# Performance work log

Hardware: AMD Instinct MI355X
Metric: run time of the kernel (lower is better)

The kernel has to match this reference:

```python
import jax, jax.numpy as jnp
import numpy as np

DEMBED = 512
DMODEL = 512
HEAD = 8
B, L = 4, 2048


def setup_inputs() -> dict:
    key = jax.random.key(0)
    ks = jax.random.split(key, 12)
    s_in = 1.0 / np.sqrt(DEMBED)
    s_out = 1.0 / np.sqrt(DMODEL)
    return {
        "x_q": jax.random.normal(ks[0], (B, L, DEMBED), jnp.float32),
        "x_k": jax.random.normal(ks[1], (B, L, DEMBED), jnp.float32),
        "x_v": jax.random.normal(ks[2], (B, L, DEMBED), jnp.float32),
        "mask": jax.random.randint(ks[3], (B, L, L), 0, 2, jnp.int32),
        "Wq": jax.random.uniform(ks[4], (DMODEL, DEMBED), jnp.float32, -s_in, s_in),
        "bq": jnp.zeros((DMODEL,), jnp.float32),
        "Wk": jax.random.uniform(ks[5], (DMODEL, DEMBED), jnp.float32, -s_in, s_in),
        "bk": jnp.zeros((DMODEL,), jnp.float32),
        "Wv": jax.random.uniform(ks[6], (DMODEL, DEMBED), jnp.float32, -s_in, s_in),
        "bv": jnp.zeros((DMODEL,), jnp.float32),
        "Wo": jax.random.uniform(ks[7], (DEMBED, DMODEL), jnp.float32, -s_out, s_out),
        "bo": jnp.zeros((DEMBED,), jnp.float32),
    }


def _split_heads(x):
    # [B, L, D] -> [B, head, L, h_dv]; head h gets contiguous channels h*h_dv:(h+1)*h_dv,
    # matching torch's transpose(1,2).reshape(B,head,h_dv,L).transpose(2,3)
    b, l, d = x.shape
    return x.reshape(b, l, HEAD, d // HEAD).transpose(0, 2, 1, 3)


def reference(x_q, x_k, x_v, mask, Wq, bq, Wk, bk, Wv, bv, Wo, bo):
    q = _split_heads(x_q @ Wq.T + bq)  # [B, H, L, hd]
    k = _split_heads(x_k @ Wk.T + bk)
    v = _split_heads(x_v @ Wv.T + bv)
    h_dv = q.shape[-1]
    scores = jnp.einsum("bhqd,bhkd->bhqk", q, k) / np.sqrt(h_dv)
    scores = scores + mask[:, None, :, :].astype(scores.dtype) * (-1e30)
    attn = jax.nn.softmax(scores, axis=-1)
    out = jnp.einsum("bhqk,bhkd->bhqd", attn, v)  # [B, H, L, hd]
    out = out.transpose(0, 2, 1, 3).reshape(x_q.shape[0], x_q.shape[1], DMODEL)
    final = out @ Wo.T + bo
    return final, attn
```

## Files before the change

kernel.cpp:

```cpp
#include <hip/hip_runtime.h>

typedef unsigned short u16;
typedef __attribute__((ext_vector_type(8))) short short8;
typedef __attribute__((ext_vector_type(4))) float f32x4;

#define DE 512
#define SL 2048
#define NB 4
#define NH 8
#define HD 64

__device__ __forceinline__ float bf2f(u16 h) {
    union { unsigned u; float f; } v; v.u = ((unsigned)h) << 16; return v.f;
}
__device__ __forceinline__ u16 f2bf(float f) {
    union { float f; unsigned u; } v; v.f = f;
    unsigned u = v.u;
    return (u16)((u + 0x7FFFu + ((u >> 16) & 1u)) >> 16);
}
__device__ __forceinline__ short8 ld8f(const float* __restrict__ p) {
    const float4 a = *(const float4*)p;
    const float4 b = *(const float4*)(p + 4);
    short8 r;
    ((u16*)&r)[0] = f2bf(a.x); ((u16*)&r)[1] = f2bf(a.y);
    ((u16*)&r)[2] = f2bf(a.z); ((u16*)&r)[3] = f2bf(a.w);
    ((u16*)&r)[4] = f2bf(b.x); ((u16*)&r)[5] = f2bf(b.y);
    ((u16*)&r)[6] = f2bf(b.z); ((u16*)&r)[7] = f2bf(b.w);
    return r;
}

__global__ __launch_bounds__(256) void cvt3(const float* __restrict__ s0,
                                            const float* __restrict__ s1,
                                            const float* __restrict__ s2,
                                            u16* __restrict__ dst, int per) {
    const float* src = (blockIdx.y == 0) ? s0 : ((blockIdx.y == 1) ? s1 : s2);
    const int idx = (blockIdx.x * 256 + threadIdx.x) * 8;
    if (idx >= per) return;
    short8 v = ld8f(src + idx);
    *(short8*)(dst + (size_t)blockIdx.y * per + idx) = v;
}

template <bool XBF, bool WBF, int MODE>
__global__ __launch_bounds__(256) void gemm512(const void* __restrict__ Xv,
                                               const void* __restrict__ Wv,
                                               const float* __restrict__ bias,
                                               void* __restrict__ outv) {
    const int lane = threadIdx.x & 63;
    const int wave = threadIdx.x >> 6;
    const int q16 = lane & 15, quad = lane >> 4;
    const int row0 = blockIdx.x * 64 + wave * 16;
    const int col0 = blockIdx.y * 64;

    f32x4 acc[4] = {};
    #pragma unroll 4
    for (int kk = 0; kk < DE; kk += 32) {
        short8 a;
        if (XBF)
            a = *(const short8*)((const u16*)Xv + (size_t)(row0 + q16) * DE + kk + quad * 8);
        else
            a = ld8f((const float*)Xv + (size_t)(row0 + q16) * DE + kk + quad * 8);
        #pragma unroll
        for (int ct = 0; ct < 4; ++ct) {
            short8 bw;
            if (WBF)
                bw = *(const short8*)((const u16*)Wv + (size_t)(col0 + ct * 16 + q16) * DE + kk + quad * 8);
            else
                bw = ld8f((const float*)Wv + (size_t)(col0 + ct * 16 + q16) * DE + kk + quad * 8);
            acc[ct] = __builtin_amdgcn_mfma_f32_16x16x32_bf16(a, bw, acc[ct], 0, 0, 0);
        }
    }

    #pragma unroll
    for (int ct = 0; ct < 4; ++ct) {
        const int col = col0 + ct * 16 + q16;
        const float bv = bias[col];
        if (MODE == 2) {
            const int tg0 = row0 + quad * 4;
            const int b = tg0 >> 11, t0 = tg0 & 2047;
            const int h = col >> 6, d = col & 63;
            ushort4 pk;
            pk.x = f2bf(acc[ct][0] + bv);
            pk.y = f2bf(acc[ct][1] + bv);
            pk.z = f2bf(acc[ct][2] + bv);
            pk.w = f2bf(acc[ct][3] + bv);
            *(ushort4*)((u16*)outv + ((size_t)((b * NH + h) * HD + d) << 11) + t0) = pk;
        } else if (MODE == 1) {
            const int h = col >> 6, d = col & 63;
            #pragma unroll
            for (int r = 0; r < 4; ++r) {
                const int tg = row0 + quad * 4 + r;
                const int b = tg >> 11, t = tg & 2047;
                ((u16*)outv)[(((size_t)(b * NH + h) * SL + t) << 6) + d] = f2bf(acc[ct][r] + bv);
            }
        } else {
            #pragma unroll
            for (int r = 0; r < 4; ++r) {
                const int tg = row0 + quad * 4 + r;
                ((float*)outv)[(size_t)tg * DE + col] = acc[ct][r] + bv;
            }
        }
    }
}

__global__ __launch_bounds__(512) void attn_kernel(const u16* __restrict__ Q,
                                                   const u16* __restrict__ K,
                                                   const u16* __restrict__ Vt,
                                                   const int* __restrict__ mask,
                                                   float* __restrict__ attn_out,
                                                   u16* __restrict__ Obuf) {
    __shared__ __align__(16) u16 P[16][2056];
    __shared__ float partial[16][8];
    __shared__ float linv[16];
    __shared__ float ored[4][16][16];

    const int tid = threadIdx.x;
    const int lane = tid & 63, wave = tid >> 6;
    const int q16 = lane & 15, quad = lane >> 4;
    const int qblk = blockIdx.x, h = blockIdx.y, b = blockIdx.z;
    const int qbase = qblk * 16;

    const u16* qplane = Q + (size_t)((b * NH + h) * SL) * HD;
    const u16* kplane = K + (size_t)((b * NH + h) * SL) * HD;

    const u16* qrow = qplane + (qbase + q16) * HD + quad * 8;
    const short8 aq0 = *(const short8*)(qrow);
    const short8 aq1 = *(const short8*)(qrow + 32);

    const int qg0 = qbase + quad * 4;
    const int* mbase = mask + (size_t)(b * SL + qg0) * SL;
    const int k0 = wave * 256;
    float rs0 = 0.f, rs1 = 0.f, rs2 = 0.f, rs3 = 0.f;
    #pragma unroll 2
    for (int kt = 0; kt < 16; ++kt) {
        const int kbase = k0 + kt * 16;
        const u16* krow = kplane + (kbase + q16) * HD + quad * 8;
        short8 b0 = *(const short8*)(krow);
        short8 b1 = *(const short8*)(krow + 32);
        f32x4 s = {};
        s = __builtin_amdgcn_mfma_f32_16x16x32_bf16(aq0, b0, s, 0, 0, 0);
        s = __builtin_amdgcn_mfma_f32_16x16x32_bf16(aq1, b1, s, 0, 0, 0);
        const int* mrow = mbase + kbase + q16;
        const float u0 = mrow[0]          ? 0.0f : __expf(s[0] * 0.125f);
        const float u1 = mrow[SL]         ? 0.0f : __expf(s[1] * 0.125f);
        const float u2 = mrow[2 * SL]     ? 0.0f : __expf(s[2] * 0.125f);
        const float u3 = mrow[3 * SL]     ? 0.0f : __expf(s[3] * 0.125f);
        rs0 += u0; rs1 += u1; rs2 += u2; rs3 += u3;
        P[quad * 4 + 0][kbase + q16] = f2bf(u0);
        P[quad * 4 + 1][kbase + q16] = f2bf(u1);
        P[quad * 4 + 2][kbase + q16] = f2bf(u2);
        P[quad * 4 + 3][kbase + q16] = f2bf(u3);
    }
    #pragma unroll
    for (int off = 1; off < 16; off <<= 1) {
        rs0 += __shfl_xor(rs0, off);
        rs1 += __shfl_xor(rs1, off);
        rs2 += __shfl_xor(rs2, off);
        rs3 += __shfl_xor(rs3, off);
    }
    if (q16 == 0) {
        partial[quad * 4 + 0][wave] = rs0;
        partial[quad * 4 + 1][wave] = rs1;
        partial[quad * 4 + 2][wave] = rs2;
        partial[quad * 4 + 3][wave] = rs3;
    }
    __syncthreads();

    if (tid < 16) {
        float s = 0.f;
        #pragma unroll
        for (int w = 0; w < 8; ++w) s += partial[tid][w];
        linv[tid] = 1.0f / s;
    }
    __syncthreads();

    {
        const int r3 = tid >> 5, cseg = tid & 31;
        const float inv = linv[r3];
        const size_t rowbase = ((size_t)((b * NH + h) * SL + qbase + r3)) * SL;
        #pragma unroll
        for (int i = 0; i < 8; ++i) {
            const int c = cseg * 8 + i * 256;
            short8 v = *(const short8*)&P[r3][c];
            f32x4 w0, w1;
            w0[0] = bf2f(((u16*)&v)[0]) * inv;
            w0[1] = bf2f(((u16*)&v)[1]) * inv;
            w0[2] = bf2f(((u16*)&v)[2]) * inv;
            w0[3] = bf2f(((u16*)&v)[3]) * inv;
            w1[0] = bf2f(((u16*)&v)[4]) * inv;
            w1[1] = bf2f(((u16*)&v)[5]) * inv;
            w1[2] = bf2f(((u16*)&v)[6]) * inv;
            w1[3] = bf2f(((u16*)&v)[7]) * inv;
            __builtin_nontemporal_store(w0, (f32x4*)(attn_out + rowbase + c));
            __builtin_nontemporal_store(w1, (f32x4*)(attn_out + rowbase + c + 4));
        }
    }

    const int dt = wave & 3, kh = wave >> 2;
    const u16* vplane = Vt + (size_t)((b * NH + h) * HD) * SL;
    f32x4 o = {};
    const int kstart = kh * 1024;
    #pragma unroll 4
    for (int kk = kstart; kk < kstart + 1024; kk += 32) {
        short8 a = *(const short8*)&P[q16][kk + quad * 8];
        short8 bv = *(const short8*)(vplane + (dt * 16 + q16) * SL + kk + quad * 8);
        o = __builtin_amdgcn_mfma_f32_16x16x32_bf16(a, bv, o, 0, 0, 0);
    }
    if (kh == 1) {
        #pragma unroll
        for (int rr = 0; rr < 4; ++rr) ored[dt][quad * 4 + rr][q16] = o[rr];
    }
    __syncthreads();
    if (kh == 0) {
        #pragma unroll
        for (int rr = 0; rr < 4; ++rr) {
            const int row = quad * 4 + rr;
            const float val = (o[rr] + ored[dt][row][q16]) * linv[row];
            const int qg = qbase + row;
            Obuf[(size_t)(b * SL + qg) * DE + h * HD + dt * 16 + q16] = f2bf(val);
        }
    }
}

extern "C" void kernel_launch(void* const* d_in, const int* in_sizes, int n_in,
                              void* d_out, int out_size, void* d_ws, size_t ws_size,
                              hipStream_t stream) {
    const float* x_q = (const float*)d_in[0];
    const float* x_k = (const float*)d_in[1];
    const float* x_v = (const float*)d_in[2];
    const int* mask = (const int*)d_in[3];
    const float* Wq = (const float*)d_in[4];
    const float* bq = (const float*)d_in[5];
    const float* Wk = (const float*)d_in[6];
    const float* bk = (const float*)d_in[7];
    const float* Wv = (const float*)d_in[8];
    const float* bv = (const float*)d_in[9];
    const float* Wo = (const float*)d_in[10];
    const float* bo = (const float*)d_in[11];

    u16* ws = (u16*)d_ws;
    u16* qb = ws;
    u16* kb = ws + 4194304;
    u16* vt = ws + 2 * 4194304;
    u16* ob = ws + 3 * 4194304;

    float* outp = (float*)d_out;
    float* attn_out = outp + 4194304;

    u16* xbf = (u16*)attn_out;
    u16* wbf = xbf + 3 * 4194304;

    cvt3<<<dim3(2048, 3), 256, 0, stream>>>(x_q, x_k, x_v, xbf, 4194304);
    cvt3<<<dim3(128, 3), 256, 0, stream>>>(Wq, Wk, Wv, wbf, 262144);

    dim3 gg(128, 8);
    gemm512<true, true, 1><<<gg, 256, 0, stream>>>(xbf, wbf, bq, qb);
    gemm512<true, true, 1><<<gg, 256, 0, stream>>>(xbf + 4194304, wbf + 262144, bk, kb);
    gemm512<true, true, 2><<<gg, 256, 0, stream>>>(xbf + 2 * 4194304, wbf + 2 * 262144, bv, vt);

    attn_kernel<<<dim3(128, 8, 4), 512, 0, stream>>>(qb, kb, vt, mask, attn_out, ob);

    if (ws_size >= (size_t)34078720) {
        u16* wobf = ws + 4 * 4194304;
        cvt3<<<dim3(128, 1), 256, 0, stream>>>(Wo, Wo, Wo, wobf, 262144);
        gemm512<true, true, 0><<<gg, 256, 0, stream>>>(ob, wobf, bo, outp);
    } else {
        gemm512<true, false, 0><<<gg, 256, 0, stream>>>(ob, Wo, bo, outp);
    }
}
```

Measured before the change: 996.0 us.

## Replace projection GEMMs with LDS-tiled double-buffered 128x128 kernel

Adds a GEMM kernel that stages 128x64 bf16 tiles of X and W into shared memory via direct global-to-LDS loads. It uses an XOR swizzle and double buffering, and each wave computes a 64x64 output block with 16 MFMA accumulators. The Q/K/V projections and the output projection now use it instead of the per-wave direct-global-load kernel, which re-read weights from global memory. This trades higher register and LDS use (one block per CU bound) for much more operand reuse.

```diff
diff --git a/kernel.cpp b/kernel.cpp
--- a/kernel.cpp
+++ b/kernel.cpp
@@ -38,6 +38,112 @@
     if (idx >= per) return;
     short8 v = ld8f(src + idx);
     *(short8*)(dst + (size_t)blockIdx.y * per + idx) = v;
+}
+
+__device__ __forceinline__ void llds16(const u16* g, u16* l) {
+    __builtin_amdgcn_global_load_lds((const __attribute__((address_space(1))) void*)g,
+                                     (__attribute__((address_space(3))) void*)l, 16, 0, 0);
+}
+
+template <int MODE>
+__global__ __launch_bounds__(256, 1) void gemm_lds(const u16* __restrict__ X,
+                                                   const u16* __restrict__ W,
+                                                   const float* __restrict__ bias,
+                                                   void* __restrict__ outv) {
+    __shared__ __align__(16) u16 As[2][8192];
+    __shared__ __align__(16) u16 Bs[2][8192];
+
+    const int tid = threadIdx.x;
+    const int l = tid & 63, w = tid >> 6;
+    const int q16 = l & 15, quad = l >> 4;
+    const int tok0 = blockIdx.x * 128;
+    const int col0 = blockIdx.y * 128;
+    const int wr = w >> 1, wc = w & 1;
+
+    const int srow = w * 8 + (l >> 3);
+    const int scol = ((l & 7) ^ (l >> 3)) * 8;
+    const u16* ga = X + (size_t)(tok0 + srow) * DE + scol;
+    const u16* gb = W + (size_t)(col0 + srow) * DE + scol;
+    u16* la0 = &As[0][tid * 8]; u16* la1 = &As[1][tid * 8];
+    u16* lb0 = &Bs[0][tid * 8]; u16* lb1 = &Bs[1][tid * 8];
+
+    f32x4 acc[4][4] = {};
+
+    #pragma unroll
+    for (int i = 0; i < 4; ++i) {
+        llds16(ga + (size_t)i * 32 * DE, la0 + i * 2048);
+        llds16(gb + (size_t)i * 32 * DE, lb0 + i * 2048);
+    }
+    __syncthreads();
+
+    int cur = 0;
+    for (int ks = 64; ks <= DE; ks += 64) {
+        if (ks < DE) {
+            u16* da = cur ? la0 : la1;
+            u16* db = cur ? lb0 : lb1;
+            #pragma unroll
+            for (int i = 0; i < 4; ++i) {
+                llds16(ga + (size_t)i * 32 * DE + ks, da + i * 2048);
+                llds16(gb + (size_t)i * 32 * DE + ks, db + i * 2048);
+            }
+        }
+        const char* Ab = (const char*)As[cur];
+        const char* Bb = (const char*)Bs[cur];
+        #pragma unroll
+        for (int kk = 0; kk < 64; kk += 32) {
+            short8 af[4], bf[4];
+            #pragma unroll
+            for (int m = 0; m < 4; ++m) {
+                const int row = wr * 64 + m * 16 + q16;
+                const int byt = row * 128 + (((kk + quad * 8) * 2) ^ ((q16 & 7) << 4));
+                af[m] = *(const short8*)(Ab + byt);
+            }
+            #pragma unroll
+            for (int n = 0; n < 4; ++n) {
+                const int row = wc * 64 + n * 16 + q16;
+                const int byt = row * 128 + (((kk + quad * 8) * 2) ^ ((q16 & 7) << 4));
+                bf[n] = *(const short8*)(Bb + byt);
+            }
+            #pragma unroll
+            for (int m = 0; m < 4; ++m)
+                #pragma unroll
+                for (int n = 0; n < 4; ++n)
+                    acc[m][n] = __builtin_amdgcn_mfma_f32_16x16x32_bf16(af[m], bf[n], acc[m][n], 0, 0, 0);
+        }
+        __syncthreads();
+        cur ^= 1;
+    }
+
+    #pragma unroll
+    for (int n = 0; n < 4; ++n) {
+        const int col = col0 + wc * 64 + n * 16 + q16;
+        const float bv = bias[col];
+        #pragma unroll
+        for (int m = 0; m < 4; ++m) {
+            const f32x4 a4 = acc[m][n];
+            const int tg0 = tok0 + wr * 64 + m * 16 + quad * 4;
+            if (MODE == 2) {
+                const int b = tg0 >> 11, t0 = tg0 & 2047;
+                const int h = col >> 6, d = col & 63;
+                ushort4 pk;
+                pk.x = f2bf(a4[0] + bv); pk.y = f2bf(a4[1] + bv);
+                pk.z = f2bf(a4[2] + bv); pk.w = f2bf(a4[3] + bv);
+                *(ushort4*)((u16*)outv + ((size_t)((b * NH + h) * HD + d) << 11) + t0) = pk;
+            } else if (MODE == 1) {
+                const int h = col >> 6, d = col & 63;
+                #pragma unroll
+                for (int r = 0; r < 4; ++r) {
+                    const int tg = tg0 + r;
+                    const int b = tg >> 11, t = tg & 2047;
+                    ((u16*)outv)[(((size_t)(b * NH + h) * SL + t) << 6) + d] = f2bf(a4[r] + bv);
+                }
+            } else {
+                #pragma unroll
+                for (int r = 0; r < 4; ++r)
+                    ((float*)outv)[(size_t)(tg0 + r) * DE + col] = a4[r] + bv;
+            }
+        }
+    }
 }
 
 template <bool XBF, bool WBF, int MODE>
@@ -69,35 +175,14 @@
             acc[ct] = __builtin_amdgcn_mfma_f32_16x16x32_bf16(a, bw, acc[ct], 0, 0, 0);
         }
     }
-
     #pragma unroll
     for (int ct = 0; ct < 4; ++ct) {
         const int col = col0 + ct * 16 + q16;
         const float bv = bias[col];
-        if (MODE == 2) {
-            const int tg0 = row0 + quad * 4;
-            const int b = tg0 >> 11, t0 = tg0 & 2047;
-            const int h = col >> 6, d = col & 63;
-            ushort4 pk;
-            pk.x = f2bf(acc[ct][0] + bv);
-            pk.y = f2bf(acc[ct][1] + bv);
-            pk.z = f2bf(acc[ct][2] + bv);
-            pk.w = f2bf(acc[ct][3] + bv);
-            *(ushort4*)((u16*)outv + ((size_t)((b * NH + h) * HD + d) << 11) + t0) = pk;
-        } else if (MODE == 1) {
-            const int h = col >> 6, d = col & 63;
-            #pragma unroll
-            for (int r = 0; r < 4; ++r) {
-                const int tg = row0 + quad * 4 + r;
-                const int b = tg >> 11, t = tg & 2047;
-                ((u16*)outv)[(((size_t)(b * NH + h) * SL + t) << 6) + d] = f2bf(acc[ct][r] + bv);
-            }
-        } else {
-            #pragma unroll
-            for (int r = 0; r < 4; ++r) {
-                const int tg = row0 + quad * 4 + r;
-                ((float*)outv)[(size_t)tg * DE + col] = acc[ct][r] + bv;
-            }
+        #pragma unroll
+        for (int r = 0; r < 4; ++r) {
+            const int tg = row0 + quad * 4 + r;
+            ((float*)outv)[(size_t)tg * DE + col] = acc[ct][r] + bv;
         }
     }
 }
@@ -252,18 +337,18 @@
     cvt3<<<dim3(2048, 3), 256, 0, stream>>>(x_q, x_k, x_v, xbf, 4194304);
     cvt3<<<dim3(128, 3), 256, 0, stream>>>(Wq, Wk, Wv, wbf, 262144);
 
-    dim3 gg(128, 8);
-    gemm512<true, true, 1><<<gg, 256, 0, stream>>>(xbf, wbf, bq, qb);
-    gemm512<true, true, 1><<<gg, 256, 0, stream>>>(xbf + 4194304, wbf + 262144, bk, kb);
-    gemm512<true, true, 2><<<gg, 256, 0, stream>>>(xbf + 2 * 4194304, wbf + 2 * 262144, bv, vt);
+    dim3 gl(64, 4);
+    gemm_lds<1><<<gl, 256, 0, stream>>>(xbf, wbf, bq, qb);
+    gemm_lds<1><<<gl, 256, 0, stream>>>(xbf + 4194304, wbf + 262144, bk, kb);
+    gemm_lds<2><<<gl, 256, 0, stream>>>(xbf + 2 * 4194304, wbf + 2 * 262144, bv, vt);
 
     attn_kernel<<<dim3(128, 8, 4), 512, 0, stream>>>(qb, kb, vt, mask, attn_out, ob);
 
     if (ws_size >= (size_t)34078720) {
         u16* wobf = ws + 4 * 4194304;
         cvt3<<<dim3(128, 1), 256, 0, stream>>>(Wo, Wo, Wo, wobf, 262144);
-        gemm512<true, true, 0><<<gg, 256, 0, stream>>>(ob, wobf, bo, outp);
+        gemm_lds<0><<<gl, 256, 0, stream>>>(ob, wobf, bo, outp);
     } else {
-        gemm512<true, false, 0><<<gg, 256, 0, stream>>>(ob, Wo, bo, outp);
-    }
-}
+        gemm512<true, false, 0><<<dim3(128, 8), 256, 0, stream>>>(ob, Wo, bo, outp);
+    }
+}
```

After: 891.0 us. 1.12x faster.
